# Kernel tuning notes

Measured on AMD Instinct MI355X. Metric: run time of the kernel, lower is better.

The kernel has to match this reference:

```python
import jax, jax.numpy as jnp
import numpy as np

B, T, C, H = 2, 2048, 1024, 16
D = C // H  # head dim = 64


def setup_inputs() -> dict:
    key = jax.random.key(0)
    ks = jax.random.split(key, 5)
    s = 0.02
    return {
        "x": jax.random.normal(ks[0], (B, T, C), dtype=jnp.float32),
        "c_attn_w": jax.random.normal(ks[1], (C, 3 * C), dtype=jnp.float32) * s,
        "c_attn_b": jax.random.normal(ks[2], (3 * C,), dtype=jnp.float32) * s,
        "c_proj_w": jax.random.normal(ks[3], (C, C), dtype=jnp.float32) * s,
        "c_proj_b": jax.random.normal(ks[4], (C,), dtype=jnp.float32) * s,
    }


def reference(x, c_attn_w, c_attn_b, c_proj_w, c_proj_b):
    b, t, c = x.shape
    # GPT-2 Conv1D: x @ W + b
    qkv = x @ c_attn_w + c_attn_b                      # [B,T,3C]
    q, k, v = jnp.split(qkv, 3, axis=-1)
    # [B,H,T,D]
    q = q.reshape(b, t, H, D).transpose(0, 2, 1, 3)
    k = k.reshape(b, t, H, D).transpose(0, 2, 1, 3)
    v = v.reshape(b, t, H, D).transpose(0, 2, 1, 3)
    scale = 1.0 / jnp.sqrt(jnp.float32(D))
    scores = jnp.einsum("bhqd,bhkd->bhqk", q, k) * scale  # [B,H,T,T]
    causal = jnp.tril(jnp.ones((t, t), dtype=bool))
    scores = jnp.where(causal, scores, jnp.float32(-jnp.inf))
    attn = jax.nn.softmax(scores, axis=-1)
    # drop_rate = 0.0 -> dropout is identity
    y = jnp.einsum("bhqk,bhkd->bhqd", attn, v)          # [B,H,T,D]
    y = y.transpose(0, 2, 1, 3).reshape(b, t, c)
    return y @ c_proj_w + c_proj_b
```

## Files before the change

### kernel.cpp

```cpp
#include <hip/hip_runtime.h>

#define B_ 2
#define T_ 2048
#define C_ 1024
#define H_ 16
#define D_ 64
#define M_ (B_ * T_)
#define NQKV_ (3 * C_)

typedef unsigned short us16;
typedef short bf16x8 __attribute__((ext_vector_type(8)));
typedef float f32x4 __attribute__((ext_vector_type(4)));

__device__ __forceinline__ f32x4 mfma16(bf16x8 a, bf16x8 b, f32x4 c) {
    return __builtin_amdgcn_mfma_f32_16x16x32_bf16(a, b, c, 0, 0, 0);
}

__device__ __forceinline__ us16 f2bf(float f) {
    union { float f; unsigned int u; } v; v.f = f;
    unsigned int r = v.u + 0x7fffu + ((v.u >> 16) & 1u);
    return (us16)(r >> 16);
}

__device__ __forceinline__ void gl_lds16(const us16* g, us16* l) {
    __builtin_amdgcn_global_load_lds(
        (const __attribute__((address_space(1))) void*)g,
        (__attribute__((address_space(3))) void*)l,
        16, 0, 0);
}

__global__ __launch_bounds__(256) void cvt_bf16(
    const float* __restrict__ in, us16* __restrict__ out, int n8)
{
    const int i = blockIdx.x * blockDim.x + threadIdx.x;
    if (i >= n8) return;
    const float4 a = ((const float4*)in)[2 * i];
    const float4 b = ((const float4*)in)[2 * i + 1];
    ushort4 lo = { f2bf(a.x), f2bf(a.y), f2bf(a.z), f2bf(a.w) };
    ushort4 hi = { f2bf(b.x), f2bf(b.y), f2bf(b.z), f2bf(b.w) };
    ((ushort4*)out)[2 * i] = lo;
    ((ushort4*)out)[2 * i + 1] = hi;
}

__global__ __launch_bounds__(256) void transpose_cvt(
    const float* __restrict__ W, us16* __restrict__ Wt, int K, int N)
{
    __shared__ float tile[32][33];
    const int n0 = blockIdx.x * 32, k0 = blockIdx.y * 32;
    const int t = threadIdx.x;
    {
        const int k = t >> 3, n4 = (t & 7) * 4;
        const float4 v = *(const float4*)(W + (size_t)(k0 + k) * N + n0 + n4);
        tile[k][n4 + 0] = v.x; tile[k][n4 + 1] = v.y;
        tile[k][n4 + 2] = v.z; tile[k][n4 + 3] = v.w;
    }
    __syncthreads();
    {
        const int n = t >> 3, k4 = (t & 7) * 4;
        ushort4 o = { f2bf(tile[k4 + 0][n]), f2bf(tile[k4 + 1][n]),
                      f2bf(tile[k4 + 2][n]), f2bf(tile[k4 + 3][n]) };
        *(ushort4*)(Wt + (size_t)(n0 + n) * K + k0 + k4) = o;
    }
}

__global__ __launch_bounds__(256) void gemm_bf16(
    const us16* __restrict__ A, const us16* __restrict__ Bt,
    const float* __restrict__ bias, void* __restrict__ Cout,
    int M, int N, int K, int out_bf16)
{
    __shared__ __align__(16) us16 smem[128 * 136];
    us16* sA = smem;
    us16* sB = smem + 128 * 64;

    const int tid = threadIdx.x;
    const int lane = tid & 63, wave = tid >> 6;
    const int wr = wave >> 1, wc = wave & 1;
    const int cq = lane & 15, quad = lane >> 4;
    const int m0 = blockIdx.y * 128, n0 = blockIdx.x * 128;

    const int srow  = lane >> 3;
    const int sgran = (lane & 7) ^ srow;
    const int scol  = sgran * 8;

    f32x4 acc[4][4];
    #pragma unroll
    for (int i = 0; i < 4; ++i)
        #pragma unroll
        for (int j = 0; j < 4; ++j)
            acc[i][j] = (f32x4){0.f, 0.f, 0.f, 0.f};

    for (int k0 = 0; k0 < K; k0 += 64) {
        #pragma unroll
        for (int p = 0; p < 4; ++p) {
            const int r = p * 32 + wave * 8;
            gl_lds16(A  + (size_t)(m0 + r + srow) * K + k0 + scol, sA + r * 64);
            gl_lds16(Bt + (size_t)(n0 + r + srow) * K + k0 + scol, sB + r * 64);
        }
        __syncthreads();

        #pragma unroll
        for (int kk = 0; kk < 64; kk += 32) {
            const int koS = (((kk >> 3) + quad) ^ (cq & 7)) << 3;
            bf16x8 af[4], bfg[4];
            #pragma unroll
            for (int i = 0; i < 4; ++i) {
                af[i]  = *(const bf16x8*)(sA + (wr * 64 + i * 16 + cq) * 64 + koS);
                bfg[i] = *(const bf16x8*)(sB + (wc * 64 + i * 16 + cq) * 64 + koS);
            }
            #pragma unroll
            for (int mi = 0; mi < 4; ++mi)
                #pragma unroll
                for (int ni = 0; ni < 4; ++ni)
                    acc[mi][ni] = mfma16(af[mi], bfg[ni], acc[mi][ni]);
        }
        __syncthreads();
    }

    if (out_bf16) {
        us16* Cs = smem;
        #pragma unroll
        for (int mi = 0; mi < 4; ++mi)
            #pragma unroll
            for (int ni = 0; ni < 4; ++ni) {
                const int n = n0 + wc * 64 + ni * 16 + cq;
                const float bv = bias[n];
                #pragma unroll
                for (int r = 0; r < 4; ++r)
                    Cs[(wr * 64 + mi * 16 + quad * 4 + r) * 136 +
                       wc * 64 + ni * 16 + cq] = f2bf(acc[mi][ni][r] + bv);
            }
        __syncthreads();
        us16* Co = (us16*)Cout;
        #pragma unroll
        for (int p = 0; p < 8; ++p) {
            const int chunk = p * 256 + tid;
            const int r = chunk >> 4, c = (chunk & 15) * 8;
            *(uint4*)(Co + (size_t)(m0 + r) * N + n0 + c) =
                *(const uint4*)(Cs + r * 136 + c);
        }
    } else {
        float* Co = (float*)Cout;
        #pragma unroll
        for (int mi = 0; mi < 4; ++mi)
            #pragma unroll
            for (int ni = 0; ni < 4; ++ni) {
                const int n = n0 + wc * 64 + ni * 16 + cq;
                const float bv = bias[n];
                #pragma unroll
                for (int r = 0; r < 4; ++r)
                    Co[(size_t)(m0 + wr * 64 + mi * 16 + quad * 4 + r) * N + n] =
                        acc[mi][ni][r] + bv;
            }
    }
}

__global__ __launch_bounds__(256) void attn_mfma(
    const us16* __restrict__ qkv, us16* __restrict__ y)
{
    __shared__ __align__(16) us16 Ks[64][72];
    __shared__ __align__(16) us16 Vt[64][72];
    __shared__ __align__(16) us16 Ps[64][72];

    const int tid = threadIdx.x;
    const int lane = tid & 63, wave = tid >> 6;
    const int cq = lane & 15, quad = lane >> 4;
    const int bh = blockIdx.x;
    const int qt = (int)gridDim.y - 1 - (int)blockIdx.y;
    const int b = bh >> 4, h = bh & 15;

    const us16* base = qkv + (size_t)b * T_ * NQKV_ + h * D_;

    bf16x8 qf[2];
    {
        const us16* qrow = base + (size_t)(qt * 64 + wave * 16 + cq) * NQKV_;
        qf[0] = *(const bf16x8*)(qrow + quad * 8);
        qf[1] = *(const bf16x8*)(qrow + 32 + quad * 8);
    }

    f32x4 ot[4];
    #pragma unroll
    for (int j = 0; j < 4; ++j) ot[j] = (f32x4){0.f, 0.f, 0.f, 0.f};
    f32x4 os = (f32x4){0.f, 0.f, 0.f, 0.f};

    const bf16x8 onesf = (bf16x8){16256, 16256, 16256, 16256,
                                  16256, 16256, 16256, 16256};

    const float ESCL = 0.125f;
    const float ESH  = -3.0f;

    const int kr0 = tid >> 3;
    const int kr1 = (256 + tid) >> 3;
    const int kc8 = (tid & 7) * 8;
    const int t2 = tid & 31, dc = tid >> 5;

    const us16* Kg = base + C_;
    const us16* Vg = base + 2 * C_;

    uint4 ka0 = *(const uint4*)(Kg + (size_t)kr0 * NQKV_ + kc8);
    uint4 ka1 = *(const uint4*)(Kg + (size_t)kr1 * NQKV_ + kc8);
    uint4 va0, va1;
    {
        const us16* vp = Vg + (size_t)(2 * t2) * NQKV_ + dc * 8;
        va0 = *(const uint4*)vp;
        va1 = *(const uint4*)(vp + NQKV_);
    }

    for (int kt = 0; kt <= qt; ++kt) {
        *(uint4*)(&Ks[kr0][kc8]) = ka0;
        *(uint4*)(&Ks[kr1][kc8]) = ka1;
        {
            const us16* p0 = (const us16*)&va0;
            const us16* p1 = (const us16*)&va1;
            #pragma unroll
            for (int j = 0; j < 8; ++j) {
                const unsigned int packed =
                    (unsigned int)p0[j] | ((unsigned int)p1[j] << 16);
                *(unsigned int*)(&Vt[dc * 8 + j][2 * t2]) = packed;
            }
        }
        __syncthreads();

        if (kt < qt) {
            const size_t ro = (size_t)((kt + 1) * 64);
            ka0 = *(const uint4*)(Kg + (ro + kr0) * NQKV_ + kc8);
            ka1 = *(const uint4*)(Kg + (ro + kr1) * NQKV_ + kc8);
            const us16* vp = Vg + (ro + 2 * t2) * NQKV_ + dc * 8;
            va0 = *(const uint4*)vp;
            va1 = *(const uint4*)(vp + NQKV_);
        }

        f32x4 s[4];
        #pragma unroll
        for (int j = 0; j < 4; ++j) {
            const bf16x8 kf0 = *(const bf16x8*)(&Ks[j * 16 + cq][quad * 8]);
            const bf16x8 kf1 = *(const bf16x8*)(&Ks[j * 16 + cq][32 + quad * 8]);
            f32x4 t = (f32x4){0.f, 0.f, 0.f, 0.f};
            t = mfma16(qf[0], kf0, t);
            t = mfma16(qf[1], kf1, t);
            s[j] = t;
        }

        float p[4][4];
        if (kt == qt) {
            const int qloc = wave * 16 + quad * 4;
            #pragma unroll
            for (int j = 0; j < 4; ++j) {
                const int kloc = j * 16 + cq;
                #pragma unroll
                for (int r = 0; r < 4; ++r) {
                    const float e = __expf(fmaf(s[j][r], ESCL, ESH));
                    p[j][r] = (kloc > qloc + r) ? 0.f : e;
                }
            }
        } else {
            #pragma unroll
            for (int j = 0; j < 4; ++j)
                #pragma unroll
                for (int r = 0; r < 4; ++r)
                    p[j][r] = __expf(fmaf(s[j][r], ESCL, ESH));
        }

        #pragma unroll
        for (int j = 0; j < 4; ++j)
            #pragma unroll
            for (int r = 0; r < 4; ++r)
                Ps[wave * 16 + quad * 4 + r][j * 16 + cq] = f2bf(p[j][r]);

        const bf16x8 pf0 = *(const bf16x8*)(&Ps[wave * 16 + cq][quad * 8]);
        const bf16x8 pf1 = *(const bf16x8*)(&Ps[wave * 16 + cq][32 + quad * 8]);

        os = mfma16(onesf, pf0, os);
        os = mfma16(onesf, pf1, os);
        #pragma unroll
        for (int dt = 0; dt < 4; ++dt) {
            const bf16x8 vf0 = *(const bf16x8*)(&Vt[dt * 16 + cq][quad * 8]);
            const bf16x8 vf1 = *(const bf16x8*)(&Vt[dt * 16 + cq][32 + quad * 8]);
            ot[dt] = mfma16(vf0, pf0, ot[dt]);
            ot[dt] = mfma16(vf1, pf1, ot[dt]);
        }

        __syncthreads();
    }

    const float inv = 1.0f / os[0];
    const int row = qt * 64 + wave * 16 + cq;
    us16* yp = y + (size_t)(b * T_ + row) * C_ + h * D_ + quad * 4;
    #pragma unroll
    for (int dt = 0; dt < 4; ++dt) {
        ushort4 ov = { f2bf(ot[dt][0] * inv), f2bf(ot[dt][1] * inv),
                       f2bf(ot[dt][2] * inv), f2bf(ot[dt][3] * inv) };
        *(ushort4*)(yp + dt * 16) = ov;
    }
}

extern "C" void kernel_launch(void* const* d_in, const int* in_sizes, int n_in,
                              void* d_out, int out_size, void* d_ws, size_t ws_size,
                              hipStream_t stream)
{
    const float* x  = (const float*)d_in[0];
    const float* aw = (const float*)d_in[1];
    const float* ab = (const float*)d_in[2];
    const float* pw = (const float*)d_in[3];
    const float* pb = (const float*)d_in[4];
    float* out = (float*)d_out;

    us16* xb   = (us16*)d_ws;
    us16* awT  = xb  + (size_t)M_ * C_;
    us16* pwT  = awT + (size_t)NQKV_ * C_;
    us16* qkvb = pwT + (size_t)C_ * C_;
    us16* yb   = qkvb + (size_t)M_ * NQKV_;

    cvt_bf16<<<(M_ * C_ / 8 + 255) / 256, 256, 0, stream>>>(x, xb, M_ * C_ / 8);
    transpose_cvt<<<dim3(NQKV_ / 32, C_ / 32), 256, 0, stream>>>(aw, awT, C_, NQKV_);
    transpose_cvt<<<dim3(C_ / 32, C_ / 32), 256, 0, stream>>>(pw, pwT, C_, C_);

    gemm_bf16<<<dim3(NQKV_ / 128, M_ / 128), 256, 0, stream>>>(
        xb, awT, ab, qkvb, M_, NQKV_, C_, 1);

    attn_mfma<<<dim3(B_ * H_, T_ / 64), 256, 0, stream>>>(qkvb, yb);

    gemm_bf16<<<dim3(C_ / 128, M_ / 128), 256, 0, stream>>>(
        yb, pwT, pb, out, M_, C_, C_, 0);
}
```

Baseline: 201.7 us.

## Double-buffer K/V tiles in LDS for attention to drop one barrier per iteration

The attention kernel now keeps two K and two transposed-V tiles in one shared-memory array. While computing on the current tile it writes the next, already-prefetched tile into the other buffer and issues global loads two tiles ahead. This removes the barrier between the LDS store and the MFMA reads in each iteration and overlaps the LDS writes with compute. The cost is roughly 46KB of LDS per block instead of about 27KB, which can lower how many blocks fit on a CU.

```diff
diff --git a/kernel.cpp b/kernel.cpp
--- a/kernel.cpp
+++ b/kernel.cpp
@@ -157,9 +157,8 @@
 __global__ __launch_bounds__(256) void attn_mfma(
     const us16* __restrict__ qkv, us16* __restrict__ y)
 {
-    __shared__ __align__(16) us16 Ks[64][72];
-    __shared__ __align__(16) us16 Vt[64][72];
-    __shared__ __align__(16) us16 Ps[64][72];
+    __shared__ __align__(16) us16 smem[5 * 64 * 72];
+    us16* Ps = smem + 4 * 4608;
 
     const int tid = threadIdx.x;
     const int lane = tid & 63, wave = tid >> 6;
@@ -204,24 +203,50 @@
         va0 = *(const uint4*)vp;
         va1 = *(const uint4*)(vp + NQKV_);
     }
+    {
+        us16* ksw = smem;
+        us16* vtw = smem + 2 * 4608;
+        *(uint4*)(ksw + kr0 * 72 + kc8) = ka0;
+        *(uint4*)(ksw + kr1 * 72 + kc8) = ka1;
+        const us16* p0 = (const us16*)&va0;
+        const us16* p1 = (const us16*)&va1;
+        #pragma unroll
+        for (int j = 0; j < 8; ++j) {
+            const unsigned int packed =
+                (unsigned int)p0[j] | ((unsigned int)p1[j] << 16);
+            *(unsigned int*)(vtw + (dc * 8 + j) * 72 + 2 * t2) = packed;
+        }
+    }
+    if (qt > 0) {
+        ka0 = *(const uint4*)(Kg + (size_t)(64 + kr0) * NQKV_ + kc8);
+        ka1 = *(const uint4*)(Kg + (size_t)(64 + kr1) * NQKV_ + kc8);
+        const us16* vp = Vg + (size_t)(64 + 2 * t2) * NQKV_ + dc * 8;
+        va0 = *(const uint4*)vp;
+        va1 = *(const uint4*)(vp + NQKV_);
+    }
+    __syncthreads();
 
     for (int kt = 0; kt <= qt; ++kt) {
-        *(uint4*)(&Ks[kr0][kc8]) = ka0;
-        *(uint4*)(&Ks[kr1][kc8]) = ka1;
-        {
+        const int cur = kt & 1;
+        const us16* ksr = smem + cur * 4608;
+        const us16* vtr = smem + (2 + cur) * 4608;
+
+        if (kt < qt) {
+            us16* ksw = smem + (cur ^ 1) * 4608;
+            us16* vtw = smem + (2 + (cur ^ 1)) * 4608;
+            *(uint4*)(ksw + kr0 * 72 + kc8) = ka0;
+            *(uint4*)(ksw + kr1 * 72 + kc8) = ka1;
             const us16* p0 = (const us16*)&va0;
             const us16* p1 = (const us16*)&va1;
             #pragma unroll
             for (int j = 0; j < 8; ++j) {
                 const unsigned int packed =
                     (unsigned int)p0[j] | ((unsigned int)p1[j] << 16);
-                *(unsigned int*)(&Vt[dc * 8 + j][2 * t2]) = packed;
-            }
-        }
-        __syncthreads();
-
-        if (kt < qt) {
-            const size_t ro = (size_t)((kt + 1) * 64);
+                *(unsigned int*)(vtw + (dc * 8 + j) * 72 + 2 * t2) = packed;
+            }
+        }
+        if (kt + 1 < qt) {
+            const size_t ro = (size_t)((kt + 2) * 64);
             ka0 = *(const uint4*)(Kg + (ro + kr0) * NQKV_ + kc8);
             ka1 = *(const uint4*)(Kg + (ro + kr1) * NQKV_ + kc8);
             const us16* vp = Vg + (ro + 2 * t2) * NQKV_ + dc * 8;
@@ -232,8 +257,8 @@
         f32x4 s[4];
         #pragma unroll
         for (int j = 0; j < 4; ++j) {
-            const bf16x8 kf0 = *(const bf16x8*)(&Ks[j * 16 + cq][quad * 8]);
-            const bf16x8 kf1 = *(const bf16x8*)(&Ks[j * 16 + cq][32 + quad * 8]);
+            const bf16x8 kf0 = *(const bf16x8*)(ksr + (j * 16 + cq) * 72 + quad * 8);
+            const bf16x8 kf1 = *(const bf16x8*)(ksr + (j * 16 + cq) * 72 + 32 + quad * 8);
             f32x4 t = (f32x4){0.f, 0.f, 0.f, 0.f};
             t = mfma16(qf[0], kf0, t);
             t = mfma16(qf[1], kf1, t);
@@ -264,17 +289,17 @@
         for (int j = 0; j < 4; ++j)
             #pragma unroll
             for (int r = 0; r < 4; ++r)
-                Ps[wave * 16 + quad * 4 + r][j * 16 + cq] = f2bf(p[j][r]);
-
-        const bf16x8 pf0 = *(const bf16x8*)(&Ps[wave * 16 + cq][quad * 8]);
-        const bf16x8 pf1 = *(const bf16x8*)(&Ps[wave * 16 + cq][32 + quad * 8]);
+                Ps[(wave * 16 + quad * 4 + r) * 72 + j * 16 + cq] = f2bf(p[j][r]);
+
+        const bf16x8 pf0 = *(const bf16x8*)(Ps + (wave * 16 + cq) * 72 + quad * 8);
+        const bf16x8 pf1 = *(const bf16x8*)(Ps + (wave * 16 + cq) * 72 + 32 + quad * 8);
 
         os = mfma16(onesf, pf0, os);
         os = mfma16(onesf, pf1, os);
         #pragma unroll
         for (int dt = 0; dt < 4; ++dt) {
-            const bf16x8 vf0 = *(const bf16x8*)(&Vt[dt * 16 + cq][quad * 8]);
-            const bf16x8 vf1 = *(const bf16x8*)(&Vt[dt * 16 + cq][32 + quad * 8]);
+            const bf16x8 vf0 = *(const bf16x8*)(vtr + (dt * 16 + cq) * 72 + quad * 8);
+            const bf16x8 vf1 = *(const bf16x8*)(vtr + (dt * 16 + cq) * 72 + 32 + quad * 8);
             ot[dt] = mfma16(vf0, pf0, ot[dt]);
             ot[dt] = mfma16(vf1, pf1, ot[dt]);
         }
```

Result: no change. 199.6 us (-1.1%).
